# Performance work log

Measured on AMD Instinct MI355X. Metric: run time of the kernel, lower is better.

## Reference

```python
import jax, jax.numpy as jnp
import numpy as np

D_MODEL = 1024
N_HEADS = 16
N_GROUPS = 4
HEAD_DIM = D_MODEL // N_HEADS          # 64
KV_HEADS = N_HEADS // N_GROUPS         # 4
D_KV = D_MODEL // N_GROUPS             # 256
B, S = 2, 2048


def setup_inputs() -> dict:
    key = jax.random.key(0)
    ks = jax.random.split(key, 10)
    sd = 1.0 / np.sqrt(D_MODEL)
    x = jax.random.normal(ks[0], (B, S, D_MODEL), dtype=jnp.float32)
    # causal mask: True means masked (matches masked_fill semantics)
    mask = jnp.triu(jnp.ones((S, S), dtype=bool), k=1)
    Wq = jax.random.normal(ks[1], (D_MODEL, D_MODEL), jnp.float32) * sd
    bq = jnp.zeros((D_MODEL,), jnp.float32)
    Wk = jax.random.normal(ks[2], (D_MODEL, D_KV), jnp.float32) * sd
    bk = jnp.zeros((D_KV,), jnp.float32)
    Wv = jax.random.normal(ks[3], (D_MODEL, D_KV), jnp.float32) * sd
    bv = jnp.zeros((D_KV,), jnp.float32)
    Wo = jax.random.normal(ks[4], (D_MODEL, D_MODEL), jnp.float32) * sd
    bo = jnp.zeros((D_MODEL,), jnp.float32)
    return {"x": x, "Wq": Wq, "bq": bq, "Wk": Wk, "bk": bk,
            "Wv": Wv, "bv": bv, "Wo": Wo, "bo": bo, "mask": mask}


def reference(x, Wq, bq, Wk, bk, Wv, bv, Wo, bo, mask):
    b, s, _ = x.shape
    scale = 1.0 / jnp.sqrt(jnp.float32(HEAD_DIM))
    # Q: [b, n_heads, s, head_dim]
    Q = (x @ Wq + bq).reshape(b, s, N_HEADS, HEAD_DIM).transpose(0, 2, 1, 3)
    # K, V: [b, kv_heads, s, head_dim]
    K = (x @ Wk + bk).reshape(b, s, KV_HEADS, HEAD_DIM).transpose(0, 2, 1, 3)
    V = (x @ Wv + bv).reshape(b, s, KV_HEADS, HEAD_DIM).transpose(0, 2, 1, 3)
    # expand: each kv head repeated n_groups consecutive times -> [b, n_heads, s, hd]
    K = jnp.repeat(K, N_GROUPS, axis=1)
    V = jnp.repeat(V, N_GROUPS, axis=1)
    scores = jnp.einsum('bhqd,bhkd->bhqk', Q, K) * scale
    scores = jnp.where(mask, -jnp.inf, scores)
    attn = jax.nn.softmax(scores, axis=-1)
    out = jnp.einsum('bhqk,bhkd->bhqd', attn, V)          # [b, h, s, hd]
    out = out.transpose(0, 2, 1, 3).reshape(b, s, D_MODEL)
    return out @ Wo + bo
```

## Files before the change

kernel.cpp:

```cpp
#include <hip/hip_runtime.h>
#include <hip/hip_bf16.h>
#include <stdint.h>

#define D_MODEL 1024
#define N_HEADS 16
#define HEAD_DIM 64
#define KV_HEADS 4
#define BATCH 2
#define SEQ 2048
#define MROWS (BATCH * SEQ)
#define NQKV 1536
#define QKV_K_OFF 1024
#define QKV_V_OFF 1280

typedef __attribute__((ext_vector_type(8))) short bf16x8;
typedef __attribute__((ext_vector_type(4))) short short4v;
typedef __attribute__((ext_vector_type(4))) float f32x4;

__device__ __forceinline__ short f2bf(float f) {
    union { float f; unsigned u; } c; c.f = f;
    unsigned u = c.u + 0x7fffu + ((c.u >> 16) & 1u);
    return (short)(u >> 16);
}
__device__ __forceinline__ unsigned pack_bf16(float a, float b) {
    return ((unsigned)(unsigned short)f2bf(a)) |
           (((unsigned)(unsigned short)f2bf(b)) << 16);
}

__global__ __launch_bounds__(256) void convert_bf16_kernel(
    const float* __restrict__ in, short* __restrict__ out, int n4)
{
    int i = blockIdx.x * 256 + threadIdx.x;
    if (i < n4) {
        float4 v = ((const float4*)in)[i];
        short4v o;
        o.x = f2bf(v.x); o.y = f2bf(v.y); o.z = f2bf(v.z); o.w = f2bf(v.w);
        ((short4v*)out)[i] = o;
    }
}

__global__ __launch_bounds__(256) void transpose_w_kernel(
    const float* __restrict__ in, int N, short* __restrict__ out)
{
    __shared__ short Ts[64][68];
    const int n0 = blockIdx.x * 64, k0 = blockIdx.y * 64;
    const int t = threadIdx.x;
    const int r = t >> 4, c4 = (t & 15) * 4;
    #pragma unroll
    for (int i = 0; i < 4; ++i) {
        int k = r + i * 16;
        float4 v = *(const float4*)(in + (size_t)(k0 + k) * N + n0 + c4);
        Ts[c4 + 0][k] = f2bf(v.x);
        Ts[c4 + 1][k] = f2bf(v.y);
        Ts[c4 + 2][k] = f2bf(v.z);
        Ts[c4 + 3][k] = f2bf(v.w);
    }
    __syncthreads();
    #pragma unroll
    for (int i = 0; i < 4; ++i) {
        int n = r + i * 16;
        short4v o = *(short4v*)&Ts[n][c4];
        *(short4v*)(out + (size_t)(n0 + n) * 1024 + k0 + c4) = o;
    }
}

__global__ __launch_bounds__(256) void bias_concat_kernel(
    const float* __restrict__ bq, const float* __restrict__ bk,
    const float* __restrict__ bv, float* __restrict__ bcat)
{
    int n = blockIdx.x * 256 + threadIdx.x;
    if (n < NQKV)
        bcat[n] = n < 1024 ? bq[n] : (n < 1280 ? bk[n - 1024] : bv[n - 1280]);
}

template <bool BF16_OUT>
__global__ __launch_bounds__(256) void gemm_kernel(
    const short* __restrict__ A, const short* __restrict__ Bt,
    const float* __restrict__ bias, void* __restrict__ Cv, int N)
{
    __shared__ short As[128 * 64];
    __shared__ short Bs[128 * 64];
    const int t = threadIdx.x;
    const int l = t & 63;
    const int w = t >> 6;
    const int bm = blockIdx.y * 128, bn = blockIdx.x * 128;
    const int wr = (w >> 1) * 64, wc = (w & 1) * 64;
    const int lr = l & 15, lg = l >> 4;

    f32x4 acc[4][4] = {};
    bf16x8 ra[4], rb[4];

    #pragma unroll
    for (int i = 0; i < 4; ++i) {
        int u = t + 256 * i, row = u >> 3, s = u & 7;
        ra[i] = *(const bf16x8*)(A  + (size_t)(bm + row) * 1024 + s * 8);
        rb[i] = *(const bf16x8*)(Bt + (size_t)(bn + row) * 1024 + s * 8);
    }

    for (int k0 = 0; k0 < 1024; k0 += 64) {
        __syncthreads();
        #pragma unroll
        for (int i = 0; i < 4; ++i) {
            int u = t + 256 * i, row = u >> 3, s = u & 7;
            int sd = s ^ (row & 7);
            *(bf16x8*)(&As[row * 64 + sd * 8]) = ra[i];
            *(bf16x8*)(&Bs[row * 64 + sd * 8]) = rb[i];
        }
        if (k0 + 64 < 1024) {
            #pragma unroll
            for (int i = 0; i < 4; ++i) {
                int u = t + 256 * i, row = u >> 3, s = u & 7;
                ra[i] = *(const bf16x8*)(A  + (size_t)(bm + row) * 1024 + k0 + 64 + s * 8);
                rb[i] = *(const bf16x8*)(Bt + (size_t)(bn + row) * 1024 + k0 + 64 + s * 8);
            }
        }
        __syncthreads();
        #pragma unroll
        for (int tt = 0; tt < 2; ++tt) {
            bf16x8 af[4], bfr[4];
            #pragma unroll
            for (int mi = 0; mi < 4; ++mi) {
                int m = wr + mi * 16 + lr;
                af[mi]  = *(const bf16x8*)(&As[m * 64 + ((tt * 4 + lg) ^ (m & 7)) * 8]);
                int n = wc + mi * 16 + lr;
                bfr[mi] = *(const bf16x8*)(&Bs[n * 64 + ((tt * 4 + lg) ^ (n & 7)) * 8]);
            }
            #pragma unroll
            for (int mi = 0; mi < 4; ++mi)
                #pragma unroll
                for (int ni = 0; ni < 4; ++ni)
                    acc[mi][ni] = __builtin_amdgcn_mfma_f32_16x16x32_bf16(
                        af[mi], bfr[ni], acc[mi][ni], 0, 0, 0);
        }
    }

    #pragma unroll
    for (int ni = 0; ni < 4; ++ni) {
        int n = bn + wc + ni * 16 + lr;
        float bv = bias[n];
        #pragma unroll
        for (int mi = 0; mi < 4; ++mi) {
            #pragma unroll
            for (int r = 0; r < 4; ++r) {
                int m = bm + wr + mi * 16 + lg * 4 + r;
                float v = acc[mi][ni][r] + bv;
                if constexpr (BF16_OUT)
                    ((short*)Cv)[(size_t)m * N + n] = f2bf(v);
                else
                    ((float*)Cv)[(size_t)m * N + n] = v;
            }
        }
    }
}

__global__ __launch_bounds__(256) void attn_kernel(
    const short* __restrict__ QKV, short* __restrict__ Aout)
{
    __shared__ short Qs[64 * 64];
    __shared__ short Ks[64 * 64];
    __shared__ short Vt[64 * 64];
    __shared__ short Ps[4 * 16 * 64];

    const int t = threadIdx.x, l = t & 63, w = t >> 6;
    const int h = blockIdx.y, b = blockIdx.z;
    const int kvh = h >> 2;
    const int lr = l & 15, lg = l >> 4;
    const float SCL = 0.125f * 1.44269504f;

    const size_t baseQ = (size_t)(b * SEQ) * NQKV + h * 64;
    const size_t baseK = (size_t)(b * SEQ) * NQKV + QKV_K_OFF + kvh * 64;
    const size_t baseV = (size_t)(b * SEQ) * NQKV + QKV_V_OFF + kvh * 64;

    for (int pi = 0; pi < 2; ++pi) {
        const int qb = pi ? (31 - (int)blockIdx.x) : (int)blockIdx.x;
        const int q0 = qb * 64;
        __syncthreads();

        #pragma unroll
        for (int i = 0; i < 2; ++i) {
            int u = t + 256 * i, row = u >> 3, s = u & 7;
            bf16x8 v = *(const bf16x8*)(QKV + baseQ + (size_t)(q0 + row) * NQKV + s * 8);
            *(bf16x8*)(&Qs[row * 64 + (s ^ (row & 7)) * 8]) = v;
        }
        bf16x8 rk[2], rv[2];
        #pragma unroll
        for (int i = 0; i < 2; ++i) {
            int u = t + 256 * i, row = u >> 3, s = u & 7;
            rk[i] = *(const bf16x8*)(QKV + baseK + (size_t)row * NQKV + s * 8);
        }
        #pragma unroll
        for (int c = 0; c < 2; ++c) {
            int d0 = (w * 2 + c) * 8;
            rv[c] = *(const bf16x8*)(QKV + baseV + (size_t)l * NQKV + d0);
        }
        __syncthreads();

        bf16x8 qf[2];
        #pragma unroll
        for (int tt = 0; tt < 2; ++tt) {
            int q = w * 16 + lr;
            qf[tt] = *(const bf16x8*)(&Qs[q * 64 + ((tt * 4 + lg) ^ (lr & 7)) * 8]);
        }

        float m_i = -INFINITY, l_i = 0.f;
        f32x4 o[4];
        #pragma unroll
        for (int ni = 0; ni < 4; ++ni) o[ni] = (f32x4){0.f, 0.f, 0.f, 0.f};

        const int qg = q0 + w * 16 + lr;

        for (int kb = 0; kb <= qb; ++kb) {
            __syncthreads();
            #pragma unroll
            for (int i = 0; i < 2; ++i) {
                int u = t + 256 * i, row = u >> 3, s = u & 7;
                *(bf16x8*)(&Ks[row * 64 + (s ^ (row & 7)) * 8]) = rk[i];
            }
            #pragma unroll
            for (int c = 0; c < 2; ++c) {
                int d0 = (w * 2 + c) * 8;
                #pragma unroll
                for (int m = 0; m < 8; ++m) {
                    int d = d0 + m;
                    Vt[d * 64 + (((l >> 3) ^ (d & 7)) * 8) + (l & 7)] = rv[c][m];
                }
            }
            if (kb < qb) {
                int kn = (kb + 1) * 64;
                #pragma unroll
                for (int i = 0; i < 2; ++i) {
                    int u = t + 256 * i, row = u >> 3, s = u & 7;
                    rk[i] = *(const bf16x8*)(QKV + baseK + (size_t)(kn + row) * NQKV + s * 8);
                }
                #pragma unroll
                for (int c = 0; c < 2; ++c) {
                    int d0 = (w * 2 + c) * 8;
                    rv[c] = *(const bf16x8*)(QKV + baseV + (size_t)(kn + l) * NQKV + d0);
                }
            }
            __syncthreads();

            f32x4 sf[4];
            #pragma unroll
            for (int ni = 0; ni < 4; ++ni) sf[ni] = (f32x4){0.f, 0.f, 0.f, 0.f};
            __builtin_amdgcn_s_setprio(1);
            #pragma unroll
            for (int tt = 0; tt < 2; ++tt) {
                #pragma unroll
                for (int ni = 0; ni < 4; ++ni) {
                    int kvr = ni * 16 + lr;
                    bf16x8 kf = *(const bf16x8*)(&Ks[kvr * 64 + ((tt * 4 + lg) ^ (lr & 7)) * 8]);
                    sf[ni] = __builtin_amdgcn_mfma_f32_16x16x32_bf16(kf, qf[tt], sf[ni], 0, 0, 0);
                }
            }
            __builtin_amdgcn_s_setprio(0);

            float p[4][4];
            #pragma unroll
            for (int ni = 0; ni < 4; ++ni)
                #pragma unroll
                for (int r = 0; r < 4; ++r)
                    p[ni][r] = sf[ni][r] * SCL;
            if (kb == qb) {
                #pragma unroll
                for (int ni = 0; ni < 4; ++ni)
                    #pragma unroll
                    for (int r = 0; r < 4; ++r)
                        if (kb * 64 + ni * 16 + lg * 4 + r > qg)
                            p[ni][r] = -INFINITY;
            }

            float rm = fmaxf(fmaxf(fmaxf(p[0][0], p[0][1]), fmaxf(p[0][2], p[0][3])),
                             fmaxf(fmaxf(p[1][0], p[1][1]), fmaxf(p[1][2], p[1][3])));
            rm = fmaxf(rm, fmaxf(fmaxf(fmaxf(p[2][0], p[2][1]), fmaxf(p[2][2], p[2][3])),
                                 fmaxf(fmaxf(p[3][0], p[3][1]), fmaxf(p[3][2], p[3][3]))));
            rm = fmaxf(rm, __shfl_xor(rm, 16));
            rm = fmaxf(rm, __shfl_xor(rm, 32));
            float mnew = fmaxf(m_i, rm);
            float corr = exp2f(m_i - mnew);
            float rs = 0.f;
            #pragma unroll
            for (int ni = 0; ni < 4; ++ni)
                #pragma unroll
                for (int r = 0; r < 4; ++r) {
                    float pv = exp2f(p[ni][r] - mnew);
                    p[ni][r] = pv;
                    rs += pv;
                }
            rs += __shfl_xor(rs, 16);
            rs += __shfl_xor(rs, 32);
            l_i = l_i * corr + rs;
            m_i = mnew;
            #pragma unroll
            for (int ni = 0; ni < 4; ++ni) o[ni] *= corr;

            #pragma unroll
            for (int ni = 0; ni < 4; ++ni) {
                int slot = (ni * 2 + (lg >> 1)) ^ (lr & 7);
                short* bp = &Ps[w * 1024 + lr * 64 + slot * 8 + (lg & 1) * 4];
                *(unsigned*)(bp)     = pack_bf16(p[ni][0], p[ni][1]);
                *(unsigned*)(bp + 2) = pack_bf16(p[ni][2], p[ni][3]);
            }

            __builtin_amdgcn_s_setprio(1);
            #pragma unroll
            for (int tt = 0; tt < 2; ++tt) {
                bf16x8 pf = *(const bf16x8*)(&Ps[w * 1024 + lr * 64 + ((tt * 4 + lg) ^ (lr & 7)) * 8]);
                #pragma unroll
                for (int ni = 0; ni < 4; ++ni) {
                    int d = ni * 16 + lr;
                    bf16x8 vf = *(const bf16x8*)(&Vt[d * 64 + ((tt * 4 + lg) ^ (lr & 7)) * 8]);
                    o[ni] = __builtin_amdgcn_mfma_f32_16x16x32_bf16(vf, pf, o[ni], 0, 0, 0);
                }
            }
            __builtin_amdgcn_s_setprio(0);
        }

        float inv = 1.0f / l_i;
        const size_t orow = (size_t)(b * SEQ + qg) * D_MODEL + h * 64;
        #pragma unroll
        for (int ni = 0; ni < 4; ++ni) {
            short4v ov;
            ov.x = f2bf(o[ni][0] * inv);
            ov.y = f2bf(o[ni][1] * inv);
            ov.z = f2bf(o[ni][2] * inv);
            ov.w = f2bf(o[ni][3] * inv);
            *(short4v*)(Aout + orow + ni * 16 + lg * 4) = ov;
        }
    }
}

extern "C" void kernel_launch(void* const* d_in, const int* in_sizes, int n_in,
                              void* d_out, int out_size, void* d_ws, size_t ws_size,
                              hipStream_t stream) {
    const float* x  = (const float*)d_in[0];
    const float* Wq = (const float*)d_in[1];
    const float* bq = (const float*)d_in[2];
    const float* Wk = (const float*)d_in[3];
    const float* bk = (const float*)d_in[4];
    const float* Wv = (const float*)d_in[5];
    const float* bv = (const float*)d_in[6];
    const float* Wo = (const float*)d_in[7];
    const float* bo = (const float*)d_in[8];
    float* out = (float*)d_out;

    short* xb    = (short*)d_ws;
    short* BtQKV = xb    + (size_t)MROWS * D_MODEL;
    short* WoT   = BtQKV + (size_t)NQKV * 1024;
    short* QKV   = WoT   + (size_t)1024 * 1024;
    short* Abuf  = QKV   + (size_t)MROWS * NQKV;
    float* bcat  = (float*)(Abuf + (size_t)MROWS * D_MODEL);

    dim3 blk(256);
    convert_bf16_kernel<<<dim3(MROWS * D_MODEL / 4 / 256), blk, 0, stream>>>(
        x, xb, MROWS * D_MODEL / 4);
    transpose_w_kernel<<<dim3(16, 16), blk, 0, stream>>>(Wq, 1024, BtQKV);
    transpose_w_kernel<<<dim3(4, 16),  blk, 0, stream>>>(Wk, 256,  BtQKV + (size_t)1024 * 1024);
    transpose_w_kernel<<<dim3(4, 16),  blk, 0, stream>>>(Wv, 256,  BtQKV + (size_t)1280 * 1024);
    transpose_w_kernel<<<dim3(16, 16), blk, 0, stream>>>(Wo, 1024, WoT);
    bias_concat_kernel<<<dim3(6), blk, 0, stream>>>(bq, bk, bv, bcat);
    gemm_kernel<true><<<dim3(NQKV / 128, MROWS / 128), blk, 0, stream>>>(
        xb, BtQKV, bcat, QKV, NQKV);
    attn_kernel<<<dim3(16, N_HEADS, BATCH), blk, 0, stream>>>(QKV, Abuf);
    gemm_kernel<false><<<dim3(D_MODEL / 128, MROWS / 128), blk, 0, stream>>>(
        Abuf, WoT, bo, out, D_MODEL);
}
```

Before: 203.6 us.

## Write V transposed from QKV GEMM, merge prep kernels, lazy softmax rescale

The QKV GEMM epilogue now writes V directly in a transposed per-kv-head layout. The attention kernel can then load V with vector loads and store it to shared memory without a scalar per-element transpose. The weight transposes and bias concat are merged into one prep launch, which cuts launch overhead. The online softmax only rescales when the running max grows by more than a threshold (a lazy-rescale trick), which saves exp and multiply work but allows larger intermediate values. The P stores are also fused into the exp loop.

```diff
diff --git a/kernel.cpp b/kernel.cpp
--- a/kernel.cpp
+++ b/kernel.cpp
@@ -9,22 +9,20 @@
 #define BATCH 2
 #define SEQ 2048
 #define MROWS (BATCH * SEQ)
-#define NQKV 1536
-#define QKV_K_OFF 1024
-#define QKV_V_OFF 1280
+#define LDQK 1280
 
 typedef __attribute__((ext_vector_type(8))) short bf16x8;
 typedef __attribute__((ext_vector_type(4))) short short4v;
 typedef __attribute__((ext_vector_type(4))) float f32x4;
 
 __device__ __forceinline__ short f2bf(float f) {
-    union { float f; unsigned u; } c; c.f = f;
-    unsigned u = c.u + 0x7fffu + ((c.u >> 16) & 1u);
-    return (short)(u >> 16);
+    __hip_bfloat16 h = __float2bfloat16(f);
+    return *reinterpret_cast<short*>(&h);
 }
 __device__ __forceinline__ unsigned pack_bf16(float a, float b) {
-    return ((unsigned)(unsigned short)f2bf(a)) |
-           (((unsigned)(unsigned short)f2bf(b)) << 16);
+    unsigned short ua = (unsigned short)f2bf(a);
+    unsigned short ub = (unsigned short)f2bf(b);
+    return (unsigned)ua | ((unsigned)ub << 16);
 }
 
 __global__ __launch_bounds__(256) void convert_bf16_kernel(
@@ -39,17 +37,39 @@
     }
 }
 
-__global__ __launch_bounds__(256) void transpose_w_kernel(
-    const float* __restrict__ in, int N, short* __restrict__ out)
+__global__ __launch_bounds__(256) void prep_kernel(
+    const float* __restrict__ Wq, const float* __restrict__ Wk,
+    const float* __restrict__ Wv, const float* __restrict__ Wo,
+    const float* __restrict__ bq, const float* __restrict__ bk,
+    const float* __restrict__ bv,
+    short* __restrict__ BtQKV, short* __restrict__ WoT,
+    float* __restrict__ bcat)
 {
+    const int z = blockIdx.z;
+    const int t = threadIdx.x;
+    if (z == 4) {
+        if (blockIdx.y == 0 && blockIdx.x < 6) {
+            int n = blockIdx.x * 256 + t;
+            bcat[n] = n < 1024 ? bq[n] : (n < 1280 ? bk[n - 1024] : bv[n - 1280]);
+        }
+        return;
+    }
+    const float* src; short* dst; int N;
+    switch (z) {
+        case 0:  src = Wq; dst = BtQKV;                       N = 1024; break;
+        case 1:  src = Wk; dst = BtQKV + (size_t)1024 * 1024; N = 256;  break;
+        case 2:  src = Wv; dst = BtQKV + (size_t)1280 * 1024; N = 256;  break;
+        default: src = Wo; dst = WoT;                         N = 1024; break;
+    }
+    const int n0 = blockIdx.x * 64;
+    if (n0 >= N) return;
+    const int k0 = blockIdx.y * 64;
     __shared__ short Ts[64][68];
-    const int n0 = blockIdx.x * 64, k0 = blockIdx.y * 64;
-    const int t = threadIdx.x;
     const int r = t >> 4, c4 = (t & 15) * 4;
     #pragma unroll
     for (int i = 0; i < 4; ++i) {
         int k = r + i * 16;
-        float4 v = *(const float4*)(in + (size_t)(k0 + k) * N + n0 + c4);
+        float4 v = *(const float4*)(src + (size_t)(k0 + k) * N + n0 + c4);
         Ts[c4 + 0][k] = f2bf(v.x);
         Ts[c4 + 1][k] = f2bf(v.y);
         Ts[c4 + 2][k] = f2bf(v.z);
@@ -60,23 +80,15 @@
     for (int i = 0; i < 4; ++i) {
         int n = r + i * 16;
         short4v o = *(short4v*)&Ts[n][c4];
-        *(short4v*)(out + (size_t)(n0 + n) * 1024 + k0 + c4) = o;
-    }
-}
-
-__global__ __launch_bounds__(256) void bias_concat_kernel(
-    const float* __restrict__ bq, const float* __restrict__ bk,
-    const float* __restrict__ bv, float* __restrict__ bcat)
-{
-    int n = blockIdx.x * 256 + threadIdx.x;
-    if (n < NQKV)
-        bcat[n] = n < 1024 ? bq[n] : (n < 1280 ? bk[n - 1024] : bv[n - 1280]);
+        *(short4v*)(dst + (size_t)(n0 + n) * 1024 + k0 + c4) = o;
+    }
 }
 
 template <bool BF16_OUT>
 __global__ __launch_bounds__(256) void gemm_kernel(
     const short* __restrict__ A, const short* __restrict__ Bt,
-    const float* __restrict__ bias, void* __restrict__ Cv, int N)
+    const float* __restrict__ bias, void* __restrict__ Cv,
+    short* __restrict__ VtG, int ldc)
 {
     __shared__ short As[128 * 64];
     __shared__ short Bs[128 * 64];
@@ -134,6 +146,28 @@
         }
     }
 
+    if constexpr (BF16_OUT) {
+        if (bn >= 1280) {
+            #pragma unroll
+            for (int ni = 0; ni < 4; ++ni) {
+                int n = bn + wc + ni * 16 + lr;
+                int vcol = n - 1280, kvh = vcol >> 6, d = vcol & 63;
+                float bv = bias[n];
+                #pragma unroll
+                for (int mi = 0; mi < 4; ++mi) {
+                    int m = bm + wr + mi * 16 + lg * 4;
+                    int b = m >> 11, kv = m & 2047;
+                    short4v ov;
+                    ov.x = f2bf(acc[mi][ni][0] + bv);
+                    ov.y = f2bf(acc[mi][ni][1] + bv);
+                    ov.z = f2bf(acc[mi][ni][2] + bv);
+                    ov.w = f2bf(acc[mi][ni][3] + bv);
+                    *(short4v*)(VtG + ((size_t)(b * 4 + kvh) * 64 + d) * 2048 + kv) = ov;
+                }
+            }
+            return;
+        }
+    }
     #pragma unroll
     for (int ni = 0; ni < 4; ++ni) {
         int n = bn + wc + ni * 16 + lr;
@@ -145,16 +179,17 @@
                 int m = bm + wr + mi * 16 + lg * 4 + r;
                 float v = acc[mi][ni][r] + bv;
                 if constexpr (BF16_OUT)
-                    ((short*)Cv)[(size_t)m * N + n] = f2bf(v);
+                    ((short*)Cv)[(size_t)m * ldc + n] = f2bf(v);
                 else
-                    ((float*)Cv)[(size_t)m * N + n] = v;
+                    ((float*)Cv)[(size_t)m * ldc + n] = v;
             }
         }
     }
 }
 
 __global__ __launch_bounds__(256) void attn_kernel(
-    const short* __restrict__ QKV, short* __restrict__ Aout)
+    const short* __restrict__ QK, const short* __restrict__ VtG,
+    short* __restrict__ Aout)
 {
     __shared__ short Qs[64 * 64];
     __shared__ short Ks[64 * 64];
@@ -167,9 +202,9 @@
     const int lr = l & 15, lg = l >> 4;
     const float SCL = 0.125f * 1.44269504f;
 
-    const size_t baseQ = (size_t)(b * SEQ) * NQKV + h * 64;
-    const size_t baseK = (size_t)(b * SEQ) * NQKV + QKV_K_OFF + kvh * 64;
-    const size_t baseV = (size_t)(b * SEQ) * NQKV + QKV_V_OFF + kvh * 64;
+    const size_t baseQ  = (size_t)(b * SEQ) * LDQK + h * 64;
+    const size_t baseK  = (size_t)(b * SEQ) * LDQK + 1024 + kvh * 64;
+    const size_t baseVt = (size_t)(b * 4 + kvh) * (64 * 2048);
 
     for (int pi = 0; pi < 2; ++pi) {
         const int qb = pi ? (31 - (int)blockIdx.x) : (int)blockIdx.x;
@@ -179,19 +214,15 @@
         #pragma unroll
         for (int i = 0; i < 2; ++i) {
             int u = t + 256 * i, row = u >> 3, s = u & 7;
-            bf16x8 v = *(const bf16x8*)(QKV + baseQ + (size_t)(q0 + row) * NQKV + s * 8);
+            bf16x8 v = *(const bf16x8*)(QK + baseQ + (size_t)(q0 + row) * LDQK + s * 8);
             *(bf16x8*)(&Qs[row * 64 + (s ^ (row & 7)) * 8]) = v;
         }
         bf16x8 rk[2], rv[2];
         #pragma unroll
         for (int i = 0; i < 2; ++i) {
             int u = t + 256 * i, row = u >> 3, s = u & 7;
-            rk[i] = *(const bf16x8*)(QKV + baseK + (size_t)row * NQKV + s * 8);
-        }
-        #pragma unroll
-        for (int c = 0; c < 2; ++c) {
-            int d0 = (w * 2 + c) * 8;
-            rv[c] = *(const bf16x8*)(QKV + baseV + (size_t)l * NQKV + d0);
+            rk[i] = *(const bf16x8*)(QK + baseK + (size_t)row * LDQK + s * 8);
+            rv[i] = *(const bf16x8*)(VtG + baseVt + (size_t)row * 2048 + s * 8);
         }
         __syncthreads();
 
@@ -215,27 +246,15 @@
             for (int i = 0; i < 2; ++i) {
                 int u = t + 256 * i, row = u >> 3, s = u & 7;
                 *(bf16x8*)(&Ks[row * 64 + (s ^ (row & 7)) * 8]) = rk[i];
-            }
-            #pragma unroll
-            for (int c = 0; c < 2; ++c) {
-                int d0 = (w * 2 + c) * 8;
-                #pragma unroll
-                for (int m = 0; m < 8; ++m) {
-                    int d = d0 + m;
-                    Vt[d * 64 + (((l >> 3) ^ (d & 7)) * 8) + (l & 7)] = rv[c][m];
-                }
+                *(bf16x8*)(&Vt[row * 64 + (s ^ (row & 7)) * 8]) = rv[i];
             }
             if (kb < qb) {
                 int kn = (kb + 1) * 64;
                 #pragma unroll
                 for (int i = 0; i < 2; ++i) {
                     int u = t + 256 * i, row = u >> 3, s = u & 7;
-                    rk[i] = *(const bf16x8*)(QKV + baseK + (size_t)(kn + row) * NQKV + s * 8);
-                }
-                #pragma unroll
-                for (int c = 0; c < 2; ++c) {
-                    int d0 = (w * 2 + c) * 8;
-                    rv[c] = *(const bf16x8*)(QKV + baseV + (size_t)(kn + l) * NQKV + d0);
+                    rk[i] = *(const bf16x8*)(QK + baseK + (size_t)(kn + row) * LDQK + s * 8);
+                    rv[i] = *(const bf16x8*)(VtG + baseVt + (size_t)row * 2048 + kn + s * 8);
                 }
             }
             __syncthreads();
@@ -276,31 +295,32 @@
                                  fmaxf(fmaxf(p[3][0], p[3][1]), fmaxf(p[3][2], p[3][3]))));
             rm = fmaxf(rm, __shfl_xor(rm, 16));
             rm = fmaxf(rm, __shfl_xor(rm, 32));
-            float mnew = fmaxf(m_i, rm);
-            float corr = exp2f(m_i - mnew);
+            if (__any(rm > m_i + 8.0f)) {
+                float mnew = fmaxf(m_i, rm);
+                float corr = exp2f(m_i - mnew);
+                l_i *= corr;
+                #pragma unroll
+                for (int ni = 0; ni < 4; ++ni) o[ni] *= corr;
+                m_i = mnew;
+            }
             float rs = 0.f;
             #pragma unroll
-            for (int ni = 0; ni < 4; ++ni)
+            for (int ni = 0; ni < 4; ++ni) {
                 #pragma unroll
                 for (int r = 0; r < 4; ++r) {
-                    float pv = exp2f(p[ni][r] - mnew);
+                    float pv = exp2f(p[ni][r] - m_i);
                     p[ni][r] = pv;
                     rs += pv;
                 }
+                int slot = (ni * 2 + (lg >> 1)) ^ (lr & 7);
+                uint2 pk;
+                pk.x = pack_bf16(p[ni][0], p[ni][1]);
+                pk.y = pack_bf16(p[ni][2], p[ni][3]);
+                *(uint2*)(&Ps[w * 1024 + lr * 64 + slot * 8 + (lg & 1) * 4]) = pk;
+            }
             rs += __shfl_xor(rs, 16);
             rs += __shfl_xor(rs, 32);
-            l_i = l_i * corr + rs;
-            m_i = mnew;
-            #pragma unroll
-            for (int ni = 0; ni < 4; ++ni) o[ni] *= corr;
-
-            #pragma unroll
-            for (int ni = 0; ni < 4; ++ni) {
-                int slot = (ni * 2 + (lg >> 1)) ^ (lr & 7);
-                short* bp = &Ps[w * 1024 + lr * 64 + slot * 8 + (lg & 1) * 4];
-                *(unsigned*)(bp)     = pack_bf16(p[ni][0], p[ni][1]);
-                *(unsigned*)(bp + 2) = pack_bf16(p[ni][2], p[ni][3]);
-            }
+            l_i += rs;
 
             __builtin_amdgcn_s_setprio(1);
             #pragma unroll
@@ -346,22 +366,20 @@
 
     short* xb    = (short*)d_ws;
     short* BtQKV = xb    + (size_t)MROWS * D_MODEL;
-    short* WoT   = BtQKV + (size_t)NQKV * 1024;
-    short* QKV   = WoT   + (size_t)1024 * 1024;
-    short* Abuf  = QKV   + (size_t)MROWS * NQKV;
+    short* WoT   = BtQKV + (size_t)1536 * 1024;
+    short* QKbuf = WoT   + (size_t)1024 * 1024;
+    short* VtG   = QKbuf + (size_t)MROWS * LDQK;
+    short* Abuf  = VtG   + (size_t)BATCH * KV_HEADS * 64 * 2048;
     float* bcat  = (float*)(Abuf + (size_t)MROWS * D_MODEL);
 
     dim3 blk(256);
     convert_bf16_kernel<<<dim3(MROWS * D_MODEL / 4 / 256), blk, 0, stream>>>(
         x, xb, MROWS * D_MODEL / 4);
-    transpose_w_kernel<<<dim3(16, 16), blk, 0, stream>>>(Wq, 1024, BtQKV);
-    transpose_w_kernel<<<dim3(4, 16),  blk, 0, stream>>>(Wk, 256,  BtQKV + (size_t)1024 * 1024);
-    transpose_w_kernel<<<dim3(4, 16),  blk, 0, stream>>>(Wv, 256,  BtQKV + (size_t)1280 * 1024);
-    transpose_w_kernel<<<dim3(16, 16), blk, 0, stream>>>(Wo, 1024, WoT);
-    bias_concat_kernel<<<dim3(6), blk, 0, stream>>>(bq, bk, bv, bcat);
-    gemm_kernel<true><<<dim3(NQKV / 128, MROWS / 128), blk, 0, stream>>>(
-        xb, BtQKV, bcat, QKV, NQKV);
-    attn_kernel<<<dim3(16, N_HEADS, BATCH), blk, 0, stream>>>(QKV, Abuf);
-    gemm_kernel<false><<<dim3(D_MODEL / 128, MROWS / 128), blk, 0, stream>>>(
-        Abuf, WoT, bo, out, D_MODEL);
-}
+    prep_kernel<<<dim3(16, 16, 5), blk, 0, stream>>>(
+        Wq, Wk, Wv, Wo, bq, bk, bv, BtQKV, WoT, bcat);
+    gemm_kernel<true><<<dim3(12, MROWS / 128), blk, 0, stream>>>(
+        xb, BtQKV, bcat, QKbuf, VtG, LDQK);
+    attn_kernel<<<dim3(16, N_HEADS, BATCH), blk, 0, stream>>>(QKbuf, VtG, Abuf);
+    gemm_kernel<false><<<dim3(8, MROWS / 128), blk, 0, stream>>>(
+        Abuf, WoT, bo, out, nullptr, 1024);
+}
```

Measured after the change: 187.9 us. 1.08x faster.
